# Optimization experiments

Hardware: AMD Instinct MI355X
Metric: run time of the kernel (lower is better)

The kernel has to match this reference:

```python
import jax, jax.numpy as jnp
import numpy as np

N_NODES = 80000
N_EDGES = 1280000
IN_CH = 128
OUT_CH = 32
HID = 2 * OUT_CH


def gcn_conv(x, W, b, src, dst, n_nodes):
    """PyG GCNConv with self-loops and symmetric normalization.
    out[i] = b + sum_{j->i} deg(j)^-1/2 deg(i)^-1/2 (x_j @ W)
    """
    loop = jnp.arange(n_nodes, dtype=src.dtype)
    s = jnp.concatenate([src, loop])  # [E+N]
    d = jnp.concatenate([dst, loop])  # [E+N]
    deg = jax.ops.segment_sum(jnp.ones_like(d, dtype=x.dtype), d,
                              num_segments=n_nodes)  # in-degree incl. self loop
    dinv = jnp.where(deg > 0, jax.lax.rsqrt(deg), 0.0)
    norm = dinv[s] * dinv[d]  # [E+N]
    h = x @ W  # [N, F_out] dense transform first (fewer flops when F_out < F_in)
    msg = h[s] * norm[:, None]  # [E+N, F_out] gather + scale
    out = jax.ops.segment_sum(msg, d, num_segments=n_nodes)  # scatter-add
    return out + b


def setup_inputs() -> dict:
    key = jax.random.key(0)
    k1, k2, k3, k4 = jax.random.split(key, 4)
    x = jax.random.normal(k1, (N_NODES, IN_CH), dtype=jnp.float32)
    edge_index = jax.random.randint(k2, (2, N_EDGES), 0, N_NODES, dtype=jnp.int64)
    W1 = jax.random.normal(k3, (IN_CH, HID), dtype=jnp.float32) / np.sqrt(IN_CH)
    b1 = jnp.zeros((HID,), dtype=jnp.float32)
    W2 = jax.random.normal(k4, (HID, OUT_CH), dtype=jnp.float32) / np.sqrt(HID)
    b2 = jnp.zeros((OUT_CH,), dtype=jnp.float32)
    return {"x": x, "edge_index": edge_index, "W1": W1, "b1": b1,
            "W2": W2, "b2": b2}


def reference(x, edge_index, W1, b1, W2, b2):
    src, dst = edge_index[0], edge_index[1]
    h = jax.nn.relu(gcn_conv(x, W1, b1, src, dst, N_NODES))
    return gcn_conv(h, W2, b2, src, dst, N_NODES)
```

## Files before the change

kernel.cpp:

```cpp
#include <hip/hip_runtime.h>
#include <hip/hip_fp16.h>

#define N_NODES 80000
#define N_EDGES 1280000
#define IN_CH 128
#define HID 64
#define OUT_CH 32

#define NBUCK 625
#define CAP 3072
#define BIN_BLOCKS 250
#define ELLW 32
#define OVF_CAP 4096

typedef float vf2 __attribute__((ext_vector_type(2)));
typedef float vf4 __attribute__((ext_vector_type(4)));
typedef short short8 __attribute__((ext_vector_type(8)));
typedef float floatx4 __attribute__((ext_vector_type(4)));

__device__ __forceinline__ unsigned bf16rn(float x) {
    unsigned u = __float_as_uint(x);
    return (u + 0x7FFFu + ((u >> 16) & 1u)) >> 16;
}
__device__ __forceinline__ unsigned packbf2(float a, float b) {
    return bf16rn(a) | (bf16rn(b) << 16);
}
__device__ __forceinline__ float hl(unsigned u) {
    return __half2float(__ushort_as_half((unsigned short)(u & 0xFFFFu)));
}
__device__ __forceinline__ float hh(unsigned u) {
    return __half2float(__ushort_as_half((unsigned short)(u >> 16)));
}
__device__ __forceinline__ unsigned pack2h(float a, float b) {
    return (unsigned)__half_as_ushort(__float2half_rn(a)) |
           ((unsigned)__half_as_ushort(__float2half_rn(b)) << 16);
}
__device__ __forceinline__ int clampid(int s) {
    unsigned v = (unsigned)s;
    return (int)(v > (unsigned)N_NODES ? (unsigned)N_NODES : v);
}

__global__ __launch_bounds__(512) void k_bin(
        const int* __restrict__ src, const int* __restrict__ dst,
        int* __restrict__ gcur, unsigned int* __restrict__ binned) {
    __shared__ int hist[NBUCK];
    __shared__ int lcur[NBUCK];
    int bid = blockIdx.x, t = threadIdx.x;
    const int chunk = N_EDGES / BIN_BLOCKS;
    int e0 = bid * chunk;
    int dv[10], sv[10];
#pragma unroll
    for (int r = 0; r < 10; ++r) {
        dv[r] = dst[e0 + t + r * 512];
        sv[r] = src[e0 + t + r * 512];
    }
    for (int i = t; i < NBUCK; i += 512) hist[i] = 0;
    __syncthreads();
#pragma unroll
    for (int r = 0; r < 10; ++r) atomicAdd(&hist[dv[r] >> 7], 1);
    __syncthreads();
    for (int i = t; i < NBUCK; i += 512) {
        int h = hist[i];
        lcur[i] = h ? atomicAdd(&gcur[i], h) : 0;
    }
    __syncthreads();
#pragma unroll
    for (int r = 0; r < 10; ++r) {
        int d = dv[r];
        int bk = d >> 7;
        int pos = atomicAdd(&lcur[bk], 1);
        if (pos < CAP)
            binned[(size_t)bk * CAP + pos] =
                (unsigned int)sv[r] | ((unsigned int)(d & 127) << 17);
    }
}

__global__ __launch_bounds__(256) void k_deg(
        const unsigned int* __restrict__ binned, const int* __restrict__ gcur,
        float2* __restrict__ meta, unsigned int* __restrict__ g2u) {
    __shared__ int deg[128];
    int bk = blockIdx.x, t = threadIdx.x;
    int n_e = min(gcur[bk], CAP);
    const unsigned int* eb = binned + (size_t)bk * CAP;
    if (bk == 0 && t < 16) g2u[(size_t)N_NODES * 16 + t] = 0u;
    if (t < 128) deg[t] = 0;
    __syncthreads();
    unsigned int pv[12];
#pragma unroll
    for (int r = 0; r < 12; ++r) {
        int i = t + r * 256;
        pv[r] = (i < n_e) ? eb[i] : 0xFFFFFFFFu;
    }
#pragma unroll
    for (int r = 0; r < 12; ++r)
        if (pv[r] != 0xFFFFFFFFu) atomicAdd(&deg[pv[r] >> 17], 1);
    __syncthreads();
    if (t < 128) {
        int dg = deg[t];
        meta[bk * 128 + t] = make_float2(rsqrtf((float)(dg + 1)), (float)dg);
    }
}

__global__ __launch_bounds__(512, 6) void k_fused(
        const unsigned int* __restrict__ binned, const int* __restrict__ gcur,
        const float2* __restrict__ meta, int* __restrict__ ell,
        int2* __restrict__ ovf, int* __restrict__ ovfcnt,
        const float* __restrict__ x, const float* __restrict__ W1,
        unsigned short* __restrict__ h1h) {
    __shared__ unsigned short smem_u[26112];
    int bid = blockIdx.x, t = threadIdx.x;
    if (bid < NBUCK) {
        int* cur = (int*)smem_u;
        int bk = bid;
        int n_e = min(gcur[bk], CAP);
        const unsigned int* eb = binned + (size_t)bk * CAP;
        if (t < 128) cur[t] = 0;
        int* eb_ell = ell + (size_t)bk * 128 * ELLW;
        for (int i = t; i < 128 * ELLW; i += 512) eb_ell[i] = N_NODES;
        unsigned int pv[6];
#pragma unroll
        for (int r = 0; r < 6; ++r) {
            int i = t + r * 512;
            pv[r] = (i < n_e) ? eb[i] : 0xFFFFFFFFu;
        }
        __syncthreads();
#pragma unroll
        for (int r = 0; r < 6; ++r) {
            unsigned int p = pv[r];
            if (p != 0xFFFFFFFFu) {
                int dL = p >> 17;
                int s = (int)(p & 0x1FFFF);
                int pos = atomicAdd(&cur[dL], 1);
                if (pos < ELLW) {
                    eb_ell[dL * ELLW + pos] = s;
                } else {
                    int o = atomicAdd(ovfcnt, 1);
                    if (o < OVF_CAP) ovf[o] = make_int2(bk * 128 + dL, s);
                }
            }
        }
    } else {
        unsigned short* sX = smem_u;
        unsigned short* sWT = smem_u + 128 * 136;
        long long nb = (long long)(bid - NBUCK) * 128;
        if (bid == NBUCK && t < 16)
            *(uint2*)&h1h[(size_t)N_NODES * 64 + t * 4] = (uint2){0u, 0u};
        {
            float4 v[8];
#pragma unroll
            for (int it = 0; it < 8; ++it) {
                int idx = t + it * 512;
                int node = idx >> 5, k4 = (idx & 31) * 4;
                v[it] = *(const float4*)&x[(nb + node) * IN_CH + k4];
            }
#pragma unroll
            for (int it = 0; it < 8; ++it) {
                int idx = t + it * 512;
                int node = idx >> 5, k4 = (idx & 31) * 4;
                *(uint2*)&sX[node * 136 + k4] =
                    (uint2){packbf2(v[it].x, v[it].y), packbf2(v[it].z, v[it].w)};
            }
        }
        {
            float4 w[4];
#pragma unroll
            for (int it = 0; it < 4; ++it) {
                int idx = t + it * 512;
                int k = idx >> 4, c4 = (idx & 15) * 4;
                w[it] = *(const float4*)&W1[k * 64 + c4];
            }
#pragma unroll
            for (int it = 0; it < 4; ++it) {
                int idx = t + it * 512;
                int k = idx >> 4, c4 = (idx & 15) * 4;
                sWT[(c4 + 0) * 136 + k] = (unsigned short)bf16rn(w[it].x);
                sWT[(c4 + 1) * 136 + k] = (unsigned short)bf16rn(w[it].y);
                sWT[(c4 + 2) * 136 + k] = (unsigned short)bf16rn(w[it].z);
                sWT[(c4 + 3) * 136 + k] = (unsigned short)bf16rn(w[it].w);
            }
        }
        __syncthreads();
        int wv = t >> 6, lane = t & 63;
        int lm = lane & 15, q = lane >> 4;
        int m0 = wv * 16;
        floatx4 acc[4];
#pragma unroll
        for (int j = 0; j < 4; ++j) acc[j] = (floatx4){0.f, 0.f, 0.f, 0.f};
#pragma unroll
        for (int kk = 0; kk < 128; kk += 32) {
            short8 a0 = *(short8*)&sX[(m0 + lm) * 136 + kk + q * 8];
#pragma unroll
            for (int ct = 0; ct < 4; ++ct) {
                short8 bfr = *(short8*)&sWT[(ct * 16 + lm) * 136 + kk + q * 8];
                acc[ct] = __builtin_amdgcn_mfma_f32_16x16x32_bf16(a0, bfr, acc[ct], 0, 0, 0);
            }
        }
        long long node0 = nb + m0 + q * 4;
        float dvr[4];
#pragma unroll
        for (int r = 0; r < 4; ++r)
            dvr[r] = meta[node0 + r].x;
#pragma unroll
        for (int ct = 0; ct < 4; ++ct)
#pragma unroll
            for (int r = 0; r < 4; ++r) {
                int c = ct * 16 + lm;
                h1h[(node0 + r) * 64 + c] =
                    __half_as_ushort(__float2half_rn(dvr[r] * acc[ct][r]));
            }
    }
}

__global__ __launch_bounds__(512) void k_agg64(
        const unsigned int* __restrict__ h1u, const int* __restrict__ ell,
        const int2* __restrict__ ovf, const int* __restrict__ ovfcnt,
        const float2* __restrict__ meta, const float* __restrict__ b1,
        const float* __restrict__ W2, unsigned int* __restrict__ g2u) {
    __shared__ float sW2[64 * 32];
    __shared__ float sH2[8][2][64];
    int t = threadIdx.x;
    for (int i = t * 2; i < 64 * 32; i += 1024)
        *(vf2*)&sW2[i] = *(const vf2*)&W2[i];

    int wv = t >> 6, lane = t & 63;
    int nd = lane >> 5;
    int q  = (lane >> 4) & 1;
    int fo = lane & 15;
    int col = lane & 31;
    int n = blockIdx.x * 16 + wv * 2 + nd;

    float2 mt = meta[n];
    float dn = mt.x;
    int dg = (int)mt.y;
    uint2 un = *(const uint2*)&h1u[(size_t)n * 32 + 2 * fo];
    float4 bb = *(const float4*)&b1[4 * fo];
    const int* er = ell + (size_t)n * ELLW;
    int4 w0 = *(const int4*)&er[0];
    int4 w1 = *(const int4*)&er[4];
    int4 w2 = *(const int4*)&er[8];
    int4 w3 = *(const int4*)&er[12];
    int4 w4 = make_int4(-1, -1, -1, -1);
    int4 w5 = w4, w6 = w4, w7 = w4;
    if (dg > 16) {
        w4 = *(const int4*)&er[16];
        w5 = *(const int4*)&er[20];
        w6 = *(const int4*)&er[24];
        w7 = *(const int4*)&er[28];
    }
    int ss[16];
    ss[0]  = q ? w0.y : w0.x;  ss[1]  = q ? w0.w : w0.z;
    ss[2]  = q ? w1.y : w1.x;  ss[3]  = q ? w1.w : w1.z;
    ss[4]  = q ? w2.y : w2.x;  ss[5]  = q ? w2.w : w2.z;
    ss[6]  = q ? w3.y : w3.x;  ss[7]  = q ? w3.w : w3.z;
    ss[8]  = q ? w4.y : w4.x;  ss[9]  = q ? w4.w : w4.z;
    ss[10] = q ? w5.y : w5.x;  ss[11] = q ? w5.w : w5.z;
    ss[12] = q ? w6.y : w6.x;  ss[13] = q ? w6.w : w6.z;
    ss[14] = q ? w7.y : w7.x;  ss[15] = q ? w7.w : w7.z;
    float ax = 0.f, ay = 0.f, az = 0.f, aw = 0.f;
#define AGG64_CHUNK(c)                                                        \
    {                                                                         \
        _Pragma("unroll")                                                     \
        for (int j = 0; j < 4; ++j) {                                         \
            int s = clampid(ss[4 * (c) + j]);                                 \
            uint2 u = *(const uint2*)&h1u[(size_t)s * 32 + 2 * fo];           \
            ax += hl(u.x); ay += hh(u.x); az += hl(u.y); aw += hh(u.y);       \
        }                                                                     \
    }
    AGG64_CHUNK(0)
    if (dg > 8)  AGG64_CHUNK(1)
    if (dg > 16) AGG64_CHUNK(2)
    if (dg > 24) AGG64_CHUNK(3)
#undef AGG64_CHUNK
    ax += __shfl_down(ax, 16); ay += __shfl_down(ay, 16);
    az += __shfl_down(az, 16); aw += __shfl_down(aw, 16);
    __syncthreads();
    if (q == 0) {
        if (dg > ELLW) {
            int m = min(ovfcnt[0], OVF_CAP);
            for (int i = 0; i < m; ++i) {
                int2 oe = ovf[i];
                if (oe.x == n) {
                    uint2 u = *(const uint2*)&h1u[(size_t)oe.y * 32 + 2 * fo];
                    ax += hl(u.x); ay += hh(u.x); az += hl(u.y); aw += hh(u.y);
                }
            }
        }
        ax += hl(un.x); ay += hh(un.x); az += hl(un.y); aw += hh(un.y);
        vf4 h2v = {fmaxf(dn * ax + bb.x, 0.f), fmaxf(dn * ay + bb.y, 0.f),
                   fmaxf(dn * az + bb.z, 0.f), fmaxf(dn * aw + bb.w, 0.f)};
        *(vf4*)&sH2[wv][nd][4 * fo] = h2v;
    }
    __syncthreads();
    int nd2 = lane >> 5;
    const float* hrow = sH2[wv][nd2];
    float g = 0.f;
#pragma unroll
    for (int k = 0; k < 64; ++k) g += hrow[k] * sW2[k * 32 + col];
    g *= dn;
    float g1 = __shfl_down(g, 1);
    float g2v = __shfl_down(g, 2);
    float g3v = __shfl_down(g, 3);
    if ((lane & 3) == 0) {
        uint2 p = {pack2h(g, g1), pack2h(g2v, g3v)};
        *(uint2*)&g2u[(size_t)n * 16 + (col >> 1)] = p;
    }
}

__global__ __launch_bounds__(256) void k_agg32(
        const unsigned int* __restrict__ g2u, const int* __restrict__ ell,
        const int2* __restrict__ ovf, const int* __restrict__ ovfcnt,
        const float2* __restrict__ meta, const float* __restrict__ b2,
        float* __restrict__ outp) {
    int n = blockIdx.x * 4 + (threadIdx.x >> 6);
    int lane = threadIdx.x & 63;
    int oc = lane >> 3, fo = lane & 7;
    float2 mt = meta[n];
    float dn = mt.x;
    int dg = (int)mt.y;
    uint2 un = *(const uint2*)&g2u[(size_t)n * 16 + 2 * fo];
    const int* er = ell + (size_t)n * ELLW;
    int s0 = er[oc];
    int s1 = er[oc + 8];
    int s2 = -1, s3 = -1;
    if (dg > 16) {
        s2 = er[oc + 16];
        s3 = er[oc + 24];
    }
    float ax = 0.f, ay = 0.f, az = 0.f, aw = 0.f;
    {
        uint2 u = *(const uint2*)&g2u[(size_t)clampid(s0) * 16 + 2 * fo];
        ax += hl(u.x); ay += hh(u.x); az += hl(u.y); aw += hh(u.y);
    }
    if (dg > 8) {
        uint2 u = *(const uint2*)&g2u[(size_t)clampid(s1) * 16 + 2 * fo];
        ax += hl(u.x); ay += hh(u.x); az += hl(u.y); aw += hh(u.y);
    }
    if (dg > 16) {
        uint2 u = *(const uint2*)&g2u[(size_t)clampid(s2) * 16 + 2 * fo];
        ax += hl(u.x); ay += hh(u.x); az += hl(u.y); aw += hh(u.y);
    }
    if (dg > 24) {
        uint2 u = *(const uint2*)&g2u[(size_t)clampid(s3) * 16 + 2 * fo];
        ax += hl(u.x); ay += hh(u.x); az += hl(u.y); aw += hh(u.y);
    }
    ax += __shfl_down(ax, 32); ay += __shfl_down(ay, 32);
    az += __shfl_down(az, 32); aw += __shfl_down(aw, 32);
    ax += __shfl_down(ax, 16); ay += __shfl_down(ay, 16);
    az += __shfl_down(az, 16); aw += __shfl_down(aw, 16);
    ax += __shfl_down(ax, 8);  ay += __shfl_down(ay, 8);
    az += __shfl_down(az, 8);  aw += __shfl_down(aw, 8);
    if (oc == 0) {
        if (dg > ELLW) {
            int m = min(ovfcnt[0], OVF_CAP);
            for (int i = 0; i < m; ++i) {
                int2 oe = ovf[i];
                if (oe.x == n) {
                    uint2 u = *(const uint2*)&g2u[(size_t)oe.y * 16 + 2 * fo];
                    ax += hl(u.x); ay += hh(u.x); az += hl(u.y); aw += hh(u.y);
                }
            }
        }
        ax += hl(un.x); ay += hh(un.x);
        az += hl(un.y); aw += hh(un.y);
        float4 bbv = *(const float4*)&b2[4 * fo];
        vf4 o = {dn * ax + bbv.x, dn * ay + bbv.y, dn * az + bbv.z, dn * aw + bbv.w};
        __builtin_nontemporal_store(o, (vf4*)&outp[(size_t)n * 32 + 4 * fo]);
    }
}

static inline size_t align256(size_t x) { return (x + 255) & ~(size_t)255; }

extern "C" void kernel_launch(void* const* d_in, const int* in_sizes, int n_in,
                              void* d_out, int out_size, void* d_ws, size_t ws_size,
                              hipStream_t stream) {
    const float* x  = (const float*)d_in[0];
    const int*   ei = (const int*)d_in[1];
    const float* W1 = (const float*)d_in[2];
    const float* b1 = (const float*)d_in[3];
    const float* W2 = (const float*)d_in[4];
    const float* b2 = (const float*)d_in[5];
    float* out = (float*)d_out;

    const int* src = ei;
    const int* dst = ei + N_EDGES;

    char* ws = (char*)d_ws;
    size_t off = 0;
    int* gcur = (int*)(ws + off);
    int* ovfcnt = gcur + NBUCK;
    off = align256(off + (size_t)(NBUCK + 1) * 4);
    int2* ovf = (int2*)(ws + off);             off = align256(off + (size_t)OVF_CAP * 8);
    unsigned int* binned = (unsigned int*)(ws + off);
                                               off = align256(off + (size_t)NBUCK * CAP * 4);
    int* ell = (int*)(ws + off);               off = align256(off + (size_t)N_NODES * ELLW * 4);
    float2* meta = (float2*)(ws + off);        off = align256(off + (size_t)N_NODES * 8);
    unsigned short* h1h = (unsigned short*)(ws + off);
                                               off = align256(off + (size_t)(N_NODES + 1) * 64 * 2);
    unsigned int* g2u = (unsigned int*)(ws + off);
                                               off = align256(off + (size_t)(N_NODES + 1) * 16 * 4);

    (void)hipMemsetAsync(gcur, 0, (size_t)(NBUCK + 1) * 4, stream);
    k_bin<<<BIN_BLOCKS, 512, 0, stream>>>(src, dst, gcur, binned);
    k_deg<<<NBUCK, 256, 0, stream>>>(binned, gcur, meta, g2u);
    k_fused<<<NBUCK + N_NODES / 128, 512, 0, stream>>>(binned, gcur, meta, ell,
                                                       ovf, ovfcnt, x, W1, h1h);
    k_agg64<<<N_NODES / 16, 512, 0, stream>>>((const unsigned int*)h1h, ell, ovf, ovfcnt,
                                              meta, b1, W2, g2u);
    k_agg32<<<N_NODES / 4, 256, 0, stream>>>(g2u, ell, ovf, ovfcnt, meta, b2, out);
}
```

Baseline: 187.9 us.

## Fuse edge binning with GEMM1 and merge degree/ELL build with dinv scaling

```diff
diff --git a/kernel.cpp b/kernel.cpp
--- a/kernel.cpp
+++ b/kernel.cpp
@@ -9,7 +9,7 @@
 
 #define NBUCK 625
 #define CAP 3072
-#define BIN_BLOCKS 250
+#define BIN_BLOCKS 128
 #define ELLW 32
 #define OVF_CAP 4096
 
@@ -40,110 +40,61 @@
     return (int)(v > (unsigned)N_NODES ? (unsigned)N_NODES : v);
 }
 
-__global__ __launch_bounds__(512) void k_bin(
+__global__ __launch_bounds__(512, 6) void k_bin_gemm1(
         const int* __restrict__ src, const int* __restrict__ dst,
-        int* __restrict__ gcur, unsigned int* __restrict__ binned) {
-    __shared__ int hist[NBUCK];
-    __shared__ int lcur[NBUCK];
-    int bid = blockIdx.x, t = threadIdx.x;
-    const int chunk = N_EDGES / BIN_BLOCKS;
-    int e0 = bid * chunk;
-    int dv[10], sv[10];
-#pragma unroll
-    for (int r = 0; r < 10; ++r) {
-        dv[r] = dst[e0 + t + r * 512];
-        sv[r] = src[e0 + t + r * 512];
-    }
-    for (int i = t; i < NBUCK; i += 512) hist[i] = 0;
-    __syncthreads();
-#pragma unroll
-    for (int r = 0; r < 10; ++r) atomicAdd(&hist[dv[r] >> 7], 1);
-    __syncthreads();
-    for (int i = t; i < NBUCK; i += 512) {
-        int h = hist[i];
-        lcur[i] = h ? atomicAdd(&gcur[i], h) : 0;
-    }
-    __syncthreads();
-#pragma unroll
-    for (int r = 0; r < 10; ++r) {
-        int d = dv[r];
-        int bk = d >> 7;
-        int pos = atomicAdd(&lcur[bk], 1);
-        if (pos < CAP)
-            binned[(size_t)bk * CAP + pos] =
-                (unsigned int)sv[r] | ((unsigned int)(d & 127) << 17);
-    }
-}
-
-__global__ __launch_bounds__(256) void k_deg(
-        const unsigned int* __restrict__ binned, const int* __restrict__ gcur,
-        float2* __restrict__ meta, unsigned int* __restrict__ g2u) {
-    __shared__ int deg[128];
-    int bk = blockIdx.x, t = threadIdx.x;
-    int n_e = min(gcur[bk], CAP);
-    const unsigned int* eb = binned + (size_t)bk * CAP;
-    if (bk == 0 && t < 16) g2u[(size_t)N_NODES * 16 + t] = 0u;
-    if (t < 128) deg[t] = 0;
-    __syncthreads();
-    unsigned int pv[12];
-#pragma unroll
-    for (int r = 0; r < 12; ++r) {
-        int i = t + r * 256;
-        pv[r] = (i < n_e) ? eb[i] : 0xFFFFFFFFu;
-    }
-#pragma unroll
-    for (int r = 0; r < 12; ++r)
-        if (pv[r] != 0xFFFFFFFFu) atomicAdd(&deg[pv[r] >> 17], 1);
-    __syncthreads();
-    if (t < 128) {
-        int dg = deg[t];
-        meta[bk * 128 + t] = make_float2(rsqrtf((float)(dg + 1)), (float)dg);
-    }
-}
-
-__global__ __launch_bounds__(512, 6) void k_fused(
-        const unsigned int* __restrict__ binned, const int* __restrict__ gcur,
-        const float2* __restrict__ meta, int* __restrict__ ell,
-        int2* __restrict__ ovf, int* __restrict__ ovfcnt,
+        int* __restrict__ gcur, unsigned int* __restrict__ binned,
         const float* __restrict__ x, const float* __restrict__ W1,
         unsigned short* __restrict__ h1h) {
     __shared__ unsigned short smem_u[26112];
     int bid = blockIdx.x, t = threadIdx.x;
-    if (bid < NBUCK) {
-        int* cur = (int*)smem_u;
-        int bk = bid;
-        int n_e = min(gcur[bk], CAP);
-        const unsigned int* eb = binned + (size_t)bk * CAP;
-        if (t < 128) cur[t] = 0;
-        int* eb_ell = ell + (size_t)bk * 128 * ELLW;
-        for (int i = t; i < 128 * ELLW; i += 512) eb_ell[i] = N_NODES;
-        unsigned int pv[6];
-#pragma unroll
-        for (int r = 0; r < 6; ++r) {
-            int i = t + r * 512;
-            pv[r] = (i < n_e) ? eb[i] : 0xFFFFFFFFu;
-        }
+    if (bid < BIN_BLOCKS) {
+        int* hist = (int*)smem_u;
+        int* lcur = hist + NBUCK;
+        const int chunk = N_EDGES / BIN_BLOCKS;
+        int e0 = bid * chunk;
+        int e1 = e0 + chunk;
+        for (int i = t; i < NBUCK; i += 512) hist[i] = 0;
         __syncthreads();
-#pragma unroll
-        for (int r = 0; r < 6; ++r) {
-            unsigned int p = pv[r];
-            if (p != 0xFFFFFFFFu) {
-                int dL = p >> 17;
-                int s = (int)(p & 0x1FFFF);
-                int pos = atomicAdd(&cur[dL], 1);
-                if (pos < ELLW) {
-                    eb_ell[dL * ELLW + pos] = s;
-                } else {
-                    int o = atomicAdd(ovfcnt, 1);
-                    if (o < OVF_CAP) ovf[o] = make_int2(bk * 128 + dL, s);
+        int dv[20];
+#pragma unroll
+        for (int r = 0; r < 20; ++r) {
+            int e = e0 + t + r * 512;
+            dv[r] = (e < e1) ? dst[e] : -1;
+        }
+#pragma unroll
+        for (int r = 0; r < 20; ++r)
+            if (dv[r] >= 0) atomicAdd(&hist[dv[r] >> 7], 1);
+        __syncthreads();
+        for (int i = t; i < NBUCK; i += 512) {
+            int h = hist[i];
+            lcur[i] = h ? atomicAdd(&gcur[i], h) : 0;
+        }
+        __syncthreads();
+#pragma unroll
+        for (int r0 = 0; r0 < 20; r0 += 4) {
+            int sv[4];
+#pragma unroll
+            for (int k = 0; k < 4; ++k) {
+                int e = e0 + t + (r0 + k) * 512;
+                sv[k] = (e < e1) ? src[e] : 0;
+            }
+#pragma unroll
+            for (int k = 0; k < 4; ++k) {
+                int d = dv[r0 + k];
+                if (d >= 0) {
+                    int bk = d >> 7;
+                    int pos = atomicAdd(&lcur[bk], 1);
+                    if (pos < CAP)
+                        binned[(size_t)bk * CAP + pos] =
+                            (unsigned int)sv[k] | ((unsigned int)(d & 127) << 17);
                 }
             }
         }
     } else {
         unsigned short* sX = smem_u;
         unsigned short* sWT = smem_u + 128 * 136;
-        long long nb = (long long)(bid - NBUCK) * 128;
-        if (bid == NBUCK && t < 16)
+        long long nb = (long long)(bid - BIN_BLOCKS) * 128;
+        if (bid == BIN_BLOCKS && t < 16)
             *(uint2*)&h1h[(size_t)N_NODES * 64 + t * 4] = (uint2){0u, 0u};
         {
             float4 v[8];
@@ -195,19 +146,74 @@
                 acc[ct] = __builtin_amdgcn_mfma_f32_16x16x32_bf16(a0, bfr, acc[ct], 0, 0, 0);
             }
         }
-        long long node0 = nb + m0 + q * 4;
-        float dvr[4];
-#pragma unroll
-        for (int r = 0; r < 4; ++r)
-            dvr[r] = meta[node0 + r].x;
 #pragma unroll
         for (int ct = 0; ct < 4; ++ct)
 #pragma unroll
             for (int r = 0; r < 4; ++r) {
+                long long node = nb + m0 + q * 4 + r;
                 int c = ct * 16 + lm;
-                h1h[(node0 + r) * 64 + c] =
-                    __half_as_ushort(__float2half_rn(dvr[r] * acc[ct][r]));
-            }
+                h1h[node * 64 + c] = __half_as_ushort(__float2half_rn(acc[ct][r]));
+            }
+    }
+}
+
+__global__ __launch_bounds__(256) void k_csr(const unsigned int* __restrict__ binned,
+                                             const int* __restrict__ gcur,
+                                             int* __restrict__ ell,
+                                             float2* __restrict__ meta,
+                                             int2* __restrict__ ovf,
+                                             int* __restrict__ ovfcnt,
+                                             unsigned int* __restrict__ h1u,
+                                             unsigned int* __restrict__ g2u) {
+    __shared__ int deg[128];
+    __shared__ int cur[128];
+    __shared__ float sdinv[128];
+    int bk = blockIdx.x, t = threadIdx.x;
+    int n_e = min(gcur[bk], CAP);
+    const unsigned int* eb = binned + (size_t)bk * CAP;
+    if (bk == 0 && t < 16) g2u[(size_t)N_NODES * 16 + t] = 0u;
+    if (t < 128) { deg[t] = 0; cur[t] = 0; }
+    int* eb_ell = ell + (size_t)bk * 128 * ELLW;
+    for (int i = t; i < 128 * ELLW; i += 256) eb_ell[i] = N_NODES;
+    unsigned int pv[12];
+#pragma unroll
+    for (int r = 0; r < 12; ++r) {
+        int i = t + r * 256;
+        pv[r] = (i < n_e) ? eb[i] : 0xFFFFFFFFu;
+    }
+    __syncthreads();
+#pragma unroll
+    for (int r = 0; r < 12; ++r) {
+        unsigned int p = pv[r];
+        if (p != 0xFFFFFFFFu) {
+            int dL = p >> 17;
+            int s = (int)(p & 0x1FFFF);
+            atomicAdd(&deg[dL], 1);
+            int pos = atomicAdd(&cur[dL], 1);
+            if (pos < ELLW) {
+                eb_ell[dL * ELLW + pos] = s;
+            } else {
+                int o = atomicAdd(ovfcnt, 1);
+                if (o < OVF_CAP) ovf[o] = make_int2(bk * 128 + dL, s);
+            }
+        }
+    }
+    __syncthreads();
+    if (t < 128) {
+        int dg = deg[t];
+        float dv = rsqrtf((float)(dg + 1));
+        sdinv[t] = dv;
+        meta[bk * 128 + t] = make_float2(dv, (float)dg);
+    }
+    __syncthreads();
+    size_t rbase = (size_t)bk * 128 * 32;
+    for (int i = t; i < 128 * 16; i += 256) {
+        int row = i >> 4, c = i & 15;
+        uint2 u = *(uint2*)&h1u[rbase + (size_t)row * 32 + 2 * c];
+        float dv = sdinv[row];
+        u.x = pack2h(dv * hl(u.x), dv * hh(u.x));
+        u.y = pack2h(dv * hl(u.y), dv * hh(u.y));
+        *(uint2*)&h1u[rbase + (size_t)row * 32 + 2 * c] = u;
     }
 }
 
@@ -400,10 +406,10 @@
                                                off = align256(off + (size_t)(N_NODES + 1) * 16 * 4);
 
     (void)hipMemsetAsync(gcur, 0, (size_t)(NBUCK + 1) * 4, stream);
-    k_bin<<<BIN_BLOCKS, 512, 0, stream>>>(src, dst, gcur, binned);
-    k_deg<<<NBUCK, 256, 0, stream>>>(binned, gcur, meta, g2u);
-    k_fused<<<NBUCK + N_NODES / 128, 512, 0, stream>>>(binned, gcur, meta, ell,
-                                                       ovf, ovfcnt, x, W1, h1h);
+    k_bin_gemm1<<<BIN_BLOCKS + N_NODES / 128, 512, 0, stream>>>(src, dst, gcur, binned,
+                                                                x, W1, h1h);
+    k_csr<<<NBUCK, 256, 0, stream>>>(binned, gcur, ell, meta, ovf, ovfcnt,
+                                     (unsigned int*)h1h, g2u);
     k_agg64<<<N_NODES / 16, 512, 0, stream>>>((const unsigned int*)h1h, ell, ovf, ovfcnt,
                                               meta, b1, W2, g2u);
     k_agg32<<<N_NODES / 4, 256, 0, stream>>>(g2u, ell, ovf, ovfcnt, meta, b2, out);
```

Measured after the change: 182.0 us. -3.1%, faster.
